# Performance work log

Hardware: AMD Instinct MI355X
Metric: run time of the kernel (lower is better)

Reference implementation:

```python
import jax, jax.numpy as jnp
import numpy as np

B, S, E, H = 2, 2048, 1024, 16
HD = E // H


def setup_inputs() -> dict:
    key = jax.random.key(0)
    ks = jax.random.split(key, 9)
    s = 1.0 / np.sqrt(E)
    return {
        "x": jax.random.normal(ks[0], (B, S, E), dtype=jnp.float32),
        "wq": jax.random.uniform(ks[1], (E, E), jnp.float32, -s, s),
        "bq": jax.random.uniform(ks[2], (E,), jnp.float32, -s, s),
        "wk": jax.random.uniform(ks[3], (E, E), jnp.float32, -s, s),
        "bk": jax.random.uniform(ks[4], (E,), jnp.float32, -s, s),
        "wv": jax.random.uniform(ks[5], (E, E), jnp.float32, -s, s),
        "bv": jax.random.uniform(ks[6], (E,), jnp.float32, -s, s),
        "wo": jax.random.uniform(ks[7], (E, E), jnp.float32, -s, s),
        "bo": jax.random.uniform(ks[8], (E,), jnp.float32, -s, s),
    }


def reference(x, wq, bq, wk, bk, wv, bv, wo, bo):
    b, s, e = x.shape
    # QKV projections, reshape to [b, h, s, hd]
    def proj(w, bias):
        y = jnp.einsum('bse,ef->bsf', x, w.T) + bias
        return y.reshape(b, s, H, HD).transpose(0, 2, 1, 3)
    q = proj(wq, bq)
    k = proj(wk, bk)
    v = proj(wv, bv)
    score = jnp.einsum('bhqd,bhkd->bhqk', q, k) / jnp.sqrt(jnp.float32(HD))
    # original: exp(x)/sum(exp(x)) + 1e-8  == softmax(x) + 1e-8
    attn = jax.nn.softmax(score, axis=-1) + 1e-8
    out = jnp.einsum('bhqk,bhkd->bhqd', attn, v)
    out = out.transpose(0, 2, 1, 3).reshape(b, s, e)
    return jnp.einsum('bse,ef->bsf', out, wo.T) + bo
```

## Files before the change

kernel.cpp:

```cpp
#include <hip/hip_runtime.h>
#include <hip/hip_bf16.h>
#include <cstdint>

#define SS 2048
#define EE 1024
#define HH 16
#define HDD 64

typedef __attribute__((ext_vector_type(8))) __bf16 bf16x8;
typedef __attribute__((ext_vector_type(4))) float f32x4;

#define MFMA16(a, b, c) __builtin_amdgcn_mfma_f32_16x16x32_bf16((a), (b), (c), 0, 0, 0)

__device__ __forceinline__ unsigned short f2bf(float f) {
    unsigned int u = __builtin_bit_cast(unsigned int, f);
    u += 0x7FFFu + ((u >> 16) & 1u);
    return (unsigned short)(u >> 16);
}

__device__ __forceinline__ void gll16(const unsigned short* g, unsigned short* l) {
    __builtin_amdgcn_global_load_lds(
        (__attribute__((address_space(1))) unsigned int*)g,
        (__attribute__((address_space(3))) unsigned int*)l, 16, 0, 0);
}

__global__ __launch_bounds__(256) void cvt_all(
    const float* __restrict__ x, const float* __restrict__ wq, const float* __restrict__ wk,
    const float* __restrict__ wv, const float* __restrict__ wo,
    unsigned short* __restrict__ xb, unsigned short* __restrict__ wqb, unsigned short* __restrict__ wkb,
    unsigned short* __restrict__ wvb, unsigned short* __restrict__ wob) {
    int idx = blockIdx.x * 256 + threadIdx.x;
    int i4 = idx << 2;
    const float* src;
    unsigned short* dst;
    int off;
    if (i4 < 4194304) { src = x; dst = xb; off = i4; }
    else {
        int w = (i4 - 4194304) >> 20;
        off = (i4 - 4194304) & 1048575;
        if (w == 0) { src = wq; dst = wqb; }
        else if (w == 1) { src = wk; dst = wkb; }
        else if (w == 2) { src = wv; dst = wvb; }
        else { src = wo; dst = wob; }
    }
    float4 v = *(const float4*)&src[off];
    unsigned int p0 = (unsigned int)f2bf(v.x) | ((unsigned int)f2bf(v.y) << 16);
    unsigned int p1 = (unsigned int)f2bf(v.z) | ((unsigned int)f2bf(v.w) << 16);
    uint2 u; u.x = p0; u.y = p1;
    *(uint2*)&dst[off] = u;
}

template <int MODE, int BNT>
__device__ __forceinline__ void gemm_core(
    const unsigned short* __restrict__ A, const unsigned short* __restrict__ W,
    const float* __restrict__ bias, void* __restrict__ out, int bm, int bn) {
    constexpr int JT = BNT / 32;
    __shared__ unsigned short lsA[128 * 32];
    __shared__ unsigned short lsB[BNT * 32];
    const int t = threadIdx.x;
    const int lane = t & 63, l15 = lane & 15, quad = lane >> 4;
    const int wave = t >> 6;
    const int wm = (wave >> 1) * 64, wn = (wave & 1) * (BNT / 2);

    const int cg = ((t & 3) ^ ((t >> 3) & 3)) * 8;
    const unsigned short* ga = A + (size_t)(bm + (t >> 2)) * 1024 + cg;
    const unsigned short* gb = W + (size_t)(bn + (t >> 2)) * 1024 + cg;

    f32x4 acc[4][JT];
    for (int i = 0; i < 4; i++)
        for (int j = 0; j < JT; j++) acc[i][j] = (f32x4){0.f, 0.f, 0.f, 0.f};

    const int swz = (l15 >> 1) & 3;

    for (int k0 = 0; k0 < 1024; k0 += 32) {
        gll16(ga + k0, &lsA[t * 8]);
        gll16(ga + k0 + 64 * 1024, &lsA[2048 + t * 8]);
        gll16(gb + k0, &lsB[t * 8]);
        if (BNT == 128) gll16(gb + k0 + 64 * 1024, &lsB[2048 + t * 8]);
        __syncthreads();
        bf16x8 af[4], bfr[JT];
        for (int i = 0; i < 4; i++)
            af[i] = *(const bf16x8*)&lsA[(wm + i * 16 + l15) * 32 + ((quad ^ swz) * 8)];
        for (int j = 0; j < JT; j++)
            bfr[j] = *(const bf16x8*)&lsB[(wn + j * 16 + l15) * 32 + ((quad ^ swz) * 8)];
        for (int i = 0; i < 4; i++)
            for (int j = 0; j < JT; j++) acc[i][j] = MFMA16(af[i], bfr[j], acc[i][j]);
        __syncthreads();
    }

    for (int j = 0; j < JT; j++) {
        int n = bn + wn + j * 16 + l15;
        float bj = bias[n];
        for (int i = 0; i < 4; i++) {
            int m0 = bm + wm + i * 16 + quad * 4;
            if (MODE == 2) {
                float v0 = acc[i][j][0] + bj, v1 = acc[i][j][1] + bj;
                float v2 = acc[i][j][2] + bj, v3 = acc[i][j][3] + bj;
                uint2 w;
                w.x = (unsigned int)f2bf(v0) | ((unsigned int)f2bf(v1) << 16);
                w.y = (unsigned int)f2bf(v2) | ((unsigned int)f2bf(v3) << 16);
                size_t addr = (((size_t)(m0 >> 11) * HH + (n >> 6)) * HDD + (n & 63)) * SS + (m0 & 2047);
                *(uint2*)&((unsigned short*)out)[addr] = w;
            } else {
                for (int rg = 0; rg < 4; rg++) {
                    float val = acc[i][j][rg] + bj;
                    int m = m0 + rg;
                    if (MODE == 0) {
                        ((unsigned short*)out)[(((size_t)(m >> 11) * HH + (n >> 6)) * SS + (m & 2047)) * HDD + (n & 63)] = f2bf(val);
                    } else {
                        ((float*)out)[(size_t)m * 1024 + n] = val;
                    }
                }
            }
        }
    }
}

__global__ __launch_bounds__(256) void gemm_qkv(
    const unsigned short* __restrict__ xb,
    const unsigned short* __restrict__ wqb, const unsigned short* __restrict__ wkb,
    const unsigned short* __restrict__ wvb,
    const float* __restrict__ bq, const float* __restrict__ bk, const float* __restrict__ bv,
    unsigned short* qb, unsigned short* kb, unsigned short* vtb) {
    const int blk = blockIdx.x;
    const int u = blk & 7, r = blk >> 3;
    const int by = u + 8 * (r & 3);
    const int rest = r >> 2;
    const int bx = rest & 7, z = rest >> 3;
    if (z == 0)      gemm_core<0, 128>(xb, wqb, bq, qb,  by * 128, bx * 128);
    else if (z == 1) gemm_core<0, 128>(xb, wkb, bk, kb,  by * 128, bx * 128);
    else             gemm_core<2, 128>(xb, wvb, bv, vtb, by * 128, bx * 128);
}

__global__ __launch_bounds__(256) void gemm_out(
    const unsigned short* __restrict__ ob, const unsigned short* __restrict__ wob,
    const float* __restrict__ bo, float* __restrict__ out) {
    const int blk = blockIdx.x;
    const int u = blk & 7, r = blk >> 3;
    const int by = u + 8 * (r & 3);
    const int bx = r >> 2;
    gemm_core<1, 64>(ob, wob, bo, out, by * 128, bx * 64);
}

#define PSTR 72

__global__ __launch_bounds__(256) void attn_fwd(
    const unsigned short* __restrict__ qb, const unsigned short* __restrict__ kb,
    const unsigned short* __restrict__ vtb, unsigned short* __restrict__ ob) {
    __shared__ unsigned short lsK[64 * 64];
    __shared__ unsigned short lsV[64 * 64];
    __shared__ unsigned short lsP[4 * 32 * PSTR];
    const int t = threadIdx.x, lane = t & 63, l15 = lane & 15, quad = lane >> 4, wave = t >> 6;
    const int blk = blockIdx.x;
    const int u = blk & 7, r = blk >> 3;
    const int bh = u + 8 * (r & 3);
    const int qt = r >> 2;
    const size_t hoff = (size_t)bh * (SS * HDD);
    const float C = 0.125f * 1.44269504088896f;

    bf16x8 qf[2][2];
    const int qrow = qt * 128 + wave * 32;
    for (int i = 0; i < 2; i++)
        for (int ks = 0; ks < 2; ks++) {
            bf16x8 raw = *(const bf16x8*)&qb[hoff + (size_t)(qrow + i * 16 + l15) * HDD + ks * 32 + quad * 8];
            unsigned short tmp[8];
            *(bf16x8*)tmp = raw;
            for (int j = 0; j < 8; j++) {
                float f = __builtin_bit_cast(float, (unsigned int)tmp[j] << 16);
                tmp[j] = f2bf(f * C);
            }
            qf[i][ks] = *(const bf16x8*)tmp;
        }

    unsigned short onesbuf[8];
    for (int j = 0; j < 8; j++) onesbuf[j] = 0x3F80;
    const bf16x8 onesf = *(const bf16x8*)onesbuf;

    f32x4 lacc[2];
    f32x4 o[2][4];
    for (int i = 0; i < 2; i++) {
        lacc[i] = (f32x4){0.f, 0.f, 0.f, 0.f};
        for (int jh = 0; jh < 4; jh++) o[i][jh] = (f32x4){0.f, 0.f, 0.f, 0.f};
    }

    const int cg = (((t & 7) ^ ((t >> 3) & 7))) * 8;
    const unsigned short* gk = kb + hoff + (size_t)(t >> 3) * HDD + cg;
    const unsigned short* gv = vtb + hoff + (size_t)(t >> 3) * SS + cg;
    const int pbase = wave * 32 * PSTR;
    const int sw = l15 & 7;

    for (int kt = 0; kt < 32; kt++) {
        gll16(gk + (size_t)kt * 64 * HDD, &lsK[t * 8]);
        gll16(gk + (size_t)kt * 64 * HDD + 32 * HDD, &lsK[2048 + t * 8]);
        gll16(gv + kt * 64, &lsV[t * 8]);
        gll16(gv + kt * 64 + 32 * SS, &lsV[2048 + t * 8]);
        __syncthreads();

        bf16x8 kfr[4][2];
        for (int j = 0; j < 4; j++)
            for (int ks = 0; ks < 2; ks++)
                kfr[j][ks] = *(const bf16x8*)&lsK[(j * 16 + l15) * 64 + (((ks * 4 + quad) ^ sw) * 8)];

        f32x4 st[4][2];
        for (int j = 0; j < 4; j++)
            for (int i = 0; i < 2; i++) {
                f32x4 z = (f32x4){0.f, 0.f, 0.f, 0.f};
                z = MFMA16(kfr[j][0], qf[i][0], z);
                z = MFMA16(kfr[j][1], qf[i][1], z);
                st[j][i] = z;
            }

        for (int j = 0; j < 4; j++)
            for (int i = 0; i < 2; i++) {
                float e0 = __builtin_amdgcn_exp2f(st[j][i][0]);
                float e1 = __builtin_amdgcn_exp2f(st[j][i][1]);
                float e2 = __builtin_amdgcn_exp2f(st[j][i][2]);
                float e3 = __builtin_amdgcn_exp2f(st[j][i][3]);
                uint2 w;
                w.x = (__builtin_bit_cast(unsigned int, e0) >> 16) |
                      (__builtin_bit_cast(unsigned int, e1) & 0xFFFF0000u);
                w.y = (__builtin_bit_cast(unsigned int, e2) >> 16) |
                      (__builtin_bit_cast(unsigned int, e3) & 0xFFFF0000u);
                *(uint2*)&lsP[pbase + (i * 16 + l15) * PSTR + j * 16 + quad * 4] = w;
            }

        bf16x8 pf[2][2], vf[4][2];
        for (int i = 0; i < 2; i++)
            for (int ks = 0; ks < 2; ks++)
                pf[i][ks] = *(const bf16x8*)&lsP[pbase + (i * 16 + l15) * PSTR + ks * 32 + quad * 8];
        for (int jh = 0; jh < 4; jh++)
            for (int ks = 0; ks < 2; ks++)
                vf[jh][ks] = *(const bf16x8*)&lsV[(jh * 16 + l15) * 64 + (((ks * 4 + quad) ^ sw) * 8)];
        for (int i = 0; i < 2; i++) {
            for (int jh = 0; jh < 4; jh++) {
                o[i][jh] = MFMA16(pf[i][0], vf[jh][0], o[i][jh]);
                o[i][jh] = MFMA16(pf[i][1], vf[jh][1], o[i][jh]);
            }
            lacc[i] = MFMA16(pf[i][0], onesf, lacc[i]);
            lacc[i] = MFMA16(pf[i][1], onesf, lacc[i]);
        }
        __syncthreads();
    }

    const int b = bh >> 4, h = bh & 15;
    for (int i = 0; i < 2; i++)
        for (int rg = 0; rg < 4; rg++) {
            float inv = 1.f / lacc[i][rg];
            int srow = qt * 128 + wave * 32 + i * 16 + quad * 4 + rg;
            size_t rowoff = ((size_t)b * SS + srow) * EE + h * 64;
            for (int jh = 0; jh < 4; jh++)
                ob[rowoff + jh * 16 + l15] = f2bf(o[i][jh][rg] * inv);
        }
}

extern "C" void kernel_launch(void* const* d_in, const int* in_sizes, int n_in,
                              void* d_out, int out_size, void* d_ws, size_t ws_size,
                              hipStream_t stream) {
    const float* x  = (const float*)d_in[0];
    const float* wq = (const float*)d_in[1];
    const float* bq = (const float*)d_in[2];
    const float* wk = (const float*)d_in[3];
    const float* bk = (const float*)d_in[4];
    const float* wv = (const float*)d_in[5];
    const float* bv = (const float*)d_in[6];
    const float* wo = (const float*)d_in[7];
    const float* bo = (const float*)d_in[8];

    char* ws = (char*)d_ws;
    unsigned short* xb  = (unsigned short*)(ws + 0);
    unsigned short* wqb = (unsigned short*)(ws + 8388608);
    unsigned short* wkb = (unsigned short*)(ws + 10485760);
    unsigned short* wvb = (unsigned short*)(ws + 12582912);
    unsigned short* wob = (unsigned short*)(ws + 14680064);
    unsigned short* qb  = (unsigned short*)(ws + 16777216);
    unsigned short* kb  = (unsigned short*)(ws + 25165824);
    unsigned short* vtb = (unsigned short*)(ws + 33554432);
    unsigned short* ob  = xb;

    cvt_all<<<8192, 256, 0, stream>>>(x, wq, wk, wv, wo, xb, wqb, wkb, wvb, wob);
    gemm_qkv<<<768, 256, 0, stream>>>(xb, wqb, wkb, wvb, bq, bk, bv, qb, kb, vtb);
    attn_fwd<<<512, 256, 0, stream>>>(qb, kb, vtb, ob);
    gemm_out<<<512, 256, 0, stream>>>(ob, wob, bo, (float*)d_out);
}
```

Measured before the change: 204.9 us.

## Store K and V in fragment-native layout and load directly to registers

The QKV GEMM now writes K and V into a pre-swizzled layout matching the MFMA fragment order, so the attention kernel can load K/V fragments straight from global memory into registers. LDS staging and both per-iteration block barriers are removed. K fragments are double-buffered in registers to prefetch the next tile, while V is loaded directly each iteration. This targets LDS traffic and synchronization cost, but it leans on L2/L1 hits for K/V reuse across the four waves and uses more registers. The K epilogue now does scalar strided stores.

Measured after the change: 215.0 us. +4.9%, slower.

```diff
diff --git a/kernel.cpp b/kernel.cpp
--- a/kernel.cpp
+++ b/kernel.cpp
@@ -93,13 +93,23 @@
         float bj = bias[n];
         for (int i = 0; i < 4; i++) {
             int m0 = bm + wm + i * 16 + quad * 4;
-            if (MODE == 2) {
+            int srow0 = m0 & 2047, bidx = m0 >> 11;
+            if (MODE == 3) {
+                size_t headb = ((size_t)bidx * HH + (n >> 6)) * (SS * HDD);
+                size_t base = headb + (size_t)(srow0 >> 6) * 4096 +
+                              (size_t)(((srow0 >> 4) & 3) * 8 + ((n & 63) >> 3)) * 128 + (n & 7);
+                for (int rg = 0; rg < 4; rg++)
+                    ((unsigned short*)out)[base + (size_t)((srow0 & 15) + rg) * 8] = f2bf(acc[i][j][rg] + bj);
+            } else if (MODE == 4) {
+                size_t headb = ((size_t)bidx * HH + (n >> 6)) * (SS * HDD);
+                size_t addr = headb + (size_t)(srow0 >> 6) * 4096 + (size_t)((n & 63) >> 4) * 1024 +
+                              (size_t)(((srow0 >> 5) & 1) * 4 + ((srow0 >> 3) & 3)) * 128 +
+                              (size_t)(n & 15) * 8 + (srow0 & 7);
                 float v0 = acc[i][j][0] + bj, v1 = acc[i][j][1] + bj;
                 float v2 = acc[i][j][2] + bj, v3 = acc[i][j][3] + bj;
                 uint2 w;
                 w.x = (unsigned int)f2bf(v0) | ((unsigned int)f2bf(v1) << 16);
                 w.y = (unsigned int)f2bf(v2) | ((unsigned int)f2bf(v3) << 16);
-                size_t addr = (((size_t)(m0 >> 11) * HH + (n >> 6)) * HDD + (n & 63)) * SS + (m0 & 2047);
                 *(uint2*)&((unsigned short*)out)[addr] = w;
             } else {
                 for (int rg = 0; rg < 4; rg++) {
@@ -128,8 +138,8 @@
     const int rest = r >> 2;
     const int bx = rest & 7, z = rest >> 3;
     if (z == 0)      gemm_core<0, 128>(xb, wqb, bq, qb,  by * 128, bx * 128);
-    else if (z == 1) gemm_core<0, 128>(xb, wkb, bk, kb,  by * 128, bx * 128);
-    else             gemm_core<2, 128>(xb, wvb, bv, vtb, by * 128, bx * 128);
+    else if (z == 1) gemm_core<3, 128>(xb, wkb, bk, kb,  by * 128, bx * 128);
+    else             gemm_core<4, 128>(xb, wvb, bv, vtb, by * 128, bx * 128);
 }
 
 __global__ __launch_bounds__(256) void gemm_out(
@@ -147,8 +157,6 @@
 __global__ __launch_bounds__(256) void attn_fwd(
     const unsigned short* __restrict__ qb, const unsigned short* __restrict__ kb,
     const unsigned short* __restrict__ vtb, unsigned short* __restrict__ ob) {
-    __shared__ unsigned short lsK[64 * 64];
-    __shared__ unsigned short lsV[64 * 64];
     __shared__ unsigned short lsP[4 * 32 * PSTR];
     const int t = threadIdx.x, lane = t & 63, l15 = lane & 15, quad = lane >> 4, wave = t >> 6;
     const int blk = blockIdx.x;
@@ -183,30 +191,34 @@
         for (int jh = 0; jh < 4; jh++) o[i][jh] = (f32x4){0.f, 0.f, 0.f, 0.f};
     }
 
-    const int cg = (((t & 7) ^ ((t >> 3) & 7))) * 8;
-    const unsigned short* gk = kb + hoff + (size_t)(t >> 3) * HDD + cg;
-    const unsigned short* gv = vtb + hoff + (size_t)(t >> 3) * SS + cg;
+    const int foff = quad * 128 + l15 * 8;
+    const unsigned short* kp = kb + hoff + foff;
+    const unsigned short* vp = vtb + hoff + foff;
     const int pbase = wave * 32 * PSTR;
-    const int sw = l15 & 7;
-
-    for (int kt = 0; kt < 32; kt++) {
-        gll16(gk + (size_t)kt * 64 * HDD, &lsK[t * 8]);
-        gll16(gk + (size_t)kt * 64 * HDD + 32 * HDD, &lsK[2048 + t * 8]);
-        gll16(gv + kt * 64, &lsV[t * 8]);
-        gll16(gv + kt * 64 + 32 * SS, &lsV[2048 + t * 8]);
-        __syncthreads();
-
-        bf16x8 kfr[4][2];
+
+    bf16x8 ka[4][2], kbuf[4][2];
+    for (int j = 0; j < 4; j++)
+        for (int ks = 0; ks < 2; ks++)
+            ka[j][ks] = *(const bf16x8*)&kp[j * 1024 + ks * 512];
+
+    auto body = [&](bf16x8 (&kc)[4][2], bf16x8 (&kn)[4][2], int kt) {
+        const unsigned short* vbase = vp + kt * 4096;
+        const unsigned short* knext = kp + ((kt + 1) & 31) * 4096;
+
+        bf16x8 vf[4][2];
+        for (int jh = 0; jh < 4; jh++)
+            for (int ks = 0; ks < 2; ks++)
+                vf[jh][ks] = *(const bf16x8*)&vbase[jh * 1024 + ks * 512];
         for (int j = 0; j < 4; j++)
             for (int ks = 0; ks < 2; ks++)
-                kfr[j][ks] = *(const bf16x8*)&lsK[(j * 16 + l15) * 64 + (((ks * 4 + quad) ^ sw) * 8)];
+                kn[j][ks] = *(const bf16x8*)&knext[j * 1024 + ks * 512];
 
         f32x4 st[4][2];
         for (int j = 0; j < 4; j++)
             for (int i = 0; i < 2; i++) {
                 f32x4 z = (f32x4){0.f, 0.f, 0.f, 0.f};
-                z = MFMA16(kfr[j][0], qf[i][0], z);
-                z = MFMA16(kfr[j][1], qf[i][1], z);
+                z = MFMA16(kc[j][0], qf[i][0], z);
+                z = MFMA16(kc[j][1], qf[i][1], z);
                 st[j][i] = z;
             }
 
@@ -224,13 +236,10 @@
                 *(uint2*)&lsP[pbase + (i * 16 + l15) * PSTR + j * 16 + quad * 4] = w;
             }
 
-        bf16x8 pf[2][2], vf[4][2];
+        bf16x8 pf[2][2];
         for (int i = 0; i < 2; i++)
             for (int ks = 0; ks < 2; ks++)
                 pf[i][ks] = *(const bf16x8*)&lsP[pbase + (i * 16 + l15) * PSTR + ks * 32 + quad * 8];
-        for (int jh = 0; jh < 4; jh++)
-            for (int ks = 0; ks < 2; ks++)
-                vf[jh][ks] = *(const bf16x8*)&lsV[(jh * 16 + l15) * 64 + (((ks * 4 + quad) ^ sw) * 8)];
         for (int i = 0; i < 2; i++) {
             for (int jh = 0; jh < 4; jh++) {
                 o[i][jh] = MFMA16(pf[i][0], vf[jh][0], o[i][jh]);
@@ -239,7 +248,11 @@
             lacc[i] = MFMA16(pf[i][0], onesf, lacc[i]);
             lacc[i] = MFMA16(pf[i][1], onesf, lacc[i]);
         }
-        __syncthreads();
+    };
+
+    for (int kt = 0; kt < 32; kt += 2) {
+        body(ka, kbuf, kt);
+        body(kbuf, ka, kt + 1);
     }
 
     const int b = bh >> 4, h = bh & 15;
```
